# Performance work log

Hardware: AMD Instinct MI355X
Metric: run time of the kernel (lower is better)

Reference implementation:

```python
import jax, jax.numpy as jnp
import numpy as np

B, S, C = 32, 512, 512      # batch, seq_len, enc_in (n_vars, used as tokens)
D, DF, H, P, PRED, K = 512, 2048, 8, 16, 96, 10


def _pe(L, d):
    # standard sinusoidal positional embedding (Informer-style)
    pos = jnp.arange(L, dtype=jnp.float32)[:, None]
    div = jnp.exp(jnp.arange(0, d, 2, dtype=jnp.float32) * (-np.log(10000.0) / d))
    pe = jnp.zeros((L, d), dtype=jnp.float32)
    pe = pe.at[:, 0::2].set(jnp.sin(pos * div))
    pe = pe.at[:, 1::2].set(jnp.cos(pos * div))
    return pe


def _pwattn(x, qw, qb, kw, kb, vw, vb, ow, ob, seq_len, pred_len):
    # patchwise attention over P-sized patches of the feature dim
    N = x.shape[0]
    query = jax.nn.relu(x @ qw + qb)                       # (N, pred_len)
    q = query.reshape(N, pred_len // P, P)
    k = (x @ kw + kb).reshape(N, seq_len // P, P)
    v = jax.nn.relu(x @ vw + vb).reshape(N, seq_len // P, P)
    A = jax.nn.softmax(jnp.einsum('ble,bse->bls', q, k) / float(np.sqrt(P)), axis=-1)
    V = jnp.einsum('bls,bse->ble', A, v).reshape(N, pred_len)
    return query + V @ ow + ob


def setup_inputs():
    key = jax.random.key(0)
    ks = iter(jax.random.split(key, 48))
    w = lambda shape: jax.random.normal(next(ks), shape, dtype=jnp.float32) * 0.02
    z = lambda n: jnp.zeros((n,), dtype=jnp.float32)
    return {
        'x_enc': jax.random.normal(next(ks), (B, S, C), dtype=jnp.float32),
        'x_mark_enc': jax.random.normal(next(ks), (B, S, 4), dtype=jnp.float32),
        'x_dec': jax.random.normal(next(ks), (B, PRED, C), dtype=jnp.float32),
        'x_mark_dec': jax.random.normal(next(ks), (B, PRED, 4), dtype=jnp.float32),
        'embed_w': w((S, D)),
        'q_w': w((D, D)), 'q_b': z(D), 'k_w': w((D, D)), 'k_b': z(D),
        'v_w': w((D, D)), 'v_b': z(D), 'o_w': w((D, D)), 'o_b': z(D),
        'enc_w': w((D, D)), 'enc_b': z(D),
        'f1q_w': w((D, DF)), 'f1q_b': z(DF), 'f1k_w': w((D, D)), 'f1k_b': z(D),
        'f1v_w': w((D, D)), 'f1v_b': z(D), 'f1o_w': w((DF, DF)), 'f1o_b': z(DF),
        'f2q_w': w((DF, D)), 'f2q_b': z(D), 'f2k_w': w((DF, DF)), 'f2k_b': z(DF),
        'f2v_w': w((DF, DF)), 'f2v_b': z(DF), 'f2o_w': w((D, D)), 'f2o_b': z(D),
        'ln_g': jnp.ones((DF,), dtype=jnp.float32), 'ln_b': z(DF),
        'fc_w': w((D, PRED)), 'fc_b': z(PRED),
    }


def reference(x_enc, x_mark_enc, x_dec, x_mark_dec, embed_w,
              q_w, q_b, k_w, k_b, v_w, v_b, o_w, o_b, enc_w, enc_b,
              f1q_w, f1q_b, f1k_w, f1k_b, f1v_w, f1v_b, f1o_w, f1o_b,
              f2q_w, f2q_b, f2k_w, f2k_b, f2v_w, f2v_b, f2o_w, f2o_b,
              ln_g, ln_b, fc_w, fc_b):
    # instance norm over time dim (stats detached)
    mean = jax.lax.stop_gradient(jnp.mean(x_enc, axis=1, keepdims=True))
    x = x_enc - mean
    std = jax.lax.stop_gradient(jnp.sqrt(jnp.var(x, axis=1, keepdims=True) + 1e-5))
    x = x / std
    x = jnp.transpose(x, (0, 2, 1))                        # (B, C, S)
    emb = jax.nn.relu(x @ embed_w) + _pe(C, D)[None]       # (B, C, D)
    # GAttn: full scores -> per-row top-k mask -> softmax -> AV
    E = D // H
    q = jax.nn.relu(emb @ q_w + q_b).reshape(B, C, H, E)
    kk = (emb @ k_w + k_b).reshape(B, C, H, E)
    v = jax.nn.relu(emb @ v_w + v_b).reshape(B, C, H, E)
    scores = jnp.einsum('blhe,bshe->bhls', q, kk)          # (B, H, C, C)
    thr = jax.lax.top_k(scores, K)[0][..., -1:]
    scores = jnp.where(scores < thr, -jnp.inf, scores)
    A = jax.nn.softmax(scores / float(np.sqrt(E)), axis=-1)
    attn_out = jnp.einsum('bhls,bshd->blhd', A, v).reshape(B, C, D)
    y = emb + (attn_out @ o_w + o_b)
    y = jax.nn.leaky_relu(y, 0.5) @ enc_w + enc_b
    y = y.reshape(B * C, D)
    # PWattn FFN with LayerNorm in between
    h = jax.nn.elu(_pwattn(y, f1q_w, f1q_b, f1k_w, f1k_b, f1v_w, f1v_b, f1o_w, f1o_b, D, DF))
    mu = jnp.mean(h, axis=-1, keepdims=True)
    var = jnp.var(h, axis=-1, keepdims=True)
    h = (h - mu) / jnp.sqrt(var + 1e-5) * ln_g + ln_b
    y = _pwattn(h, f2q_w, f2q_b, f2k_w, f2k_b, f2v_w, f2v_b, f2o_w, f2o_b, DF, D)
    y = y.reshape(B, C, D)
    dec = y @ fc_w + fc_b                                   # (B, C, PRED)
    dec = jnp.transpose(dec, (0, 2, 1))                     # (B, PRED, C)
    dec = dec * std + mean
    return dec[:, -PRED:, :]
```

## Files before the change

### kernel.cpp

```cpp
#include <hip/hip_runtime.h>
#include <float.h>
#include <math.h>
#include <stdint.h>


#define NB   32
#define SS   512
#define CC   512
#define DD   512
#define DFF  2048
#define HH   8
#define EE   64
#define PRED 96

typedef __attribute__((ext_vector_type(8))) short short8;
typedef __attribute__((ext_vector_type(4))) float f32x4;

__device__ __forceinline__ float b2f(ushort u) {
  union { float f; uint32_t i; } c; c.i = ((uint32_t)u) << 16; return c.f;
}
__device__ __forceinline__ ushort f2b(float f) {
  union { float f; uint32_t i; } c; c.f = f;
  uint32_t x = c.i;
  return (ushort)((x + 0x7fffu + ((x >> 16) & 1u)) >> 16);
}
__device__ __forceinline__ float lin(const void* p, size_t i, int f32) {
  return f32 ? ((const float*)p)[i] : b2f(((const ushort*)p)[i]);
}
__device__ __forceinline__ void split_bf(float x, ushort& hi, ushort& lo) {
  hi = f2b(x);
  lo = f2b(x - b2f(hi));
}

template<int CTRL>
__device__ __forceinline__ float dppmov(float x) {
  union { float f; int i; } a, b;
  a.f = x;
  b.i = __builtin_amdgcn_update_dpp(a.i, a.i, CTRL, 0xF, 0xF, false);
  return b.f;
}
__device__ __forceinline__ float red16_max(float x) {
  x = fmaxf(x, dppmov<0xB1>(x));
  x = fmaxf(x, dppmov<0x4E>(x));
  x = fmaxf(x, dppmov<0x141>(x));
  x = fmaxf(x, dppmov<0x140>(x));
  return x;
}
__device__ __forceinline__ float red16_sum(float x) {
  x += dppmov<0xB1>(x);
  x += dppmov<0x4E>(x);
  x += dppmov<0x141>(x);
  x += dppmov<0x140>(x);
  return x;
}

__global__ __launch_bounds__(256) void detect_dtype(
    const ushort* __restrict__ x, int* __restrict__ flag)
{
  __shared__ float red[256];
  const int t = threadIdx.x;
  float v = fabsf(b2f(x[2 * t]));
  if (!(v < 1e30f)) v = 1e30f;
  red[t] = v;
  __syncthreads();
  for (int off = 128; off > 0; off >>= 1) {
    if (t < off) red[t] = fmaxf(red[t], red[t + off]);
    __syncthreads();
  }
  if (t == 0) flag[0] = (red[0] > 1e6f) ? 1 : 0;
}

__global__ __launch_bounds__(256) void instnorm_stats(
    const void* __restrict__ x, float* __restrict__ meanb, float* __restrict__ stdb,
    const int* __restrict__ dtf)
{
  const int f32 = *dtf;
  const int c = blockIdx.x * 256 + threadIdx.x;
  const int b = blockIdx.y;
  float s = 0.f, s2 = 0.f;
  for (int t = 0; t < SS; ++t) {
    const float xv = lin(x, ((size_t)(b * SS) + t) * CC + c, f32);
    s += xv; s2 += xv * xv;
  }
  const float mu  = s * (1.f / SS);
  const float var = s2 * (1.f / SS) - mu * mu;
  meanb[b * CC + c] = mu;
  stdb [b * CC + c] = sqrtf(var + 1e-5f);
}

__global__ __launch_bounds__(256) void norm_transpose(
    const void* __restrict__ x, const float* __restrict__ meanb,
    const float* __restrict__ stdb, float* __restrict__ xTc, int b_base,
    const int* __restrict__ dtf)
{
  const int f32 = *dtf;
  __shared__ float t[32][33];
  const int s0 = blockIdx.x * 32, c0 = blockIdx.y * 32, lb = blockIdx.z;
  const int b = b_base + lb;
  const int tx = threadIdx.x & 31, ty = threadIdx.x >> 5;
  #pragma unroll
  for (int i = 0; i < 4; ++i) {
    const int s = s0 + ty + i * 8;
    t[ty + i * 8][tx] = lin(x, ((size_t)(b * SS) + s) * CC + c0 + tx, f32);
  }
  __syncthreads();
  #pragma unroll
  for (int i = 0; i < 4; ++i) {
    const int c = c0 + ty + i * 8;
    const float mu = meanb[b * CC + c], sd = stdb[b * CC + c];
    xTc[((size_t)(lb * CC) + c) * SS + s0 + tx] = (t[tx][ty + i * 8] - mu) / sd;
  }
}

__global__ __launch_bounds__(256) void norm_transpose_split(
    const void* __restrict__ x, const float* __restrict__ meanb,
    const float* __restrict__ stdb, ushort* __restrict__ xh,
    ushort* __restrict__ xl, int b_base, const int* __restrict__ dtf)
{
  const int f32 = *dtf;
  __shared__ float t[32][33];
  const int s0 = blockIdx.x * 32, c0 = blockIdx.y * 32, lb = blockIdx.z;
  const int b = b_base + lb;
  const int tx = threadIdx.x & 31, ty = threadIdx.x >> 5;
  #pragma unroll
  for (int i = 0; i < 4; ++i) {
    const int s = s0 + ty + i * 8;
    t[ty + i * 8][tx] = lin(x, ((size_t)(b * SS) + s) * CC + c0 + tx, f32);
  }
  __syncthreads();
  #pragma unroll
  for (int i = 0; i < 4; ++i) {
    const int c = c0 + ty + i * 8;
    const float mu = meanb[b * CC + c], sd = stdb[b * CC + c];
    const float v = (t[tx][ty + i * 8] - mu) / sd;
    const size_t idx = ((size_t)(lb * CC) + c) * SS + s0 + tx;
    ushort hi, lo; split_bf(v, hi, lo);
    xh[idx] = hi; xl[idx] = lo;
  }
}

__global__ __launch_bounds__(256) void transpose_w(
    const void* __restrict__ W, ushort* __restrict__ Wt, int K, int N,
    const int* __restrict__ dtf)
{
  const int f32 = *dtf;
  __shared__ float t[32][33];
  const int n0 = blockIdx.x * 32, k0 = blockIdx.y * 32;
  const int tx = threadIdx.x & 31, ty = threadIdx.x >> 5;
  #pragma unroll
  for (int i = 0; i < 4; ++i)
    t[ty + i * 8][tx] = lin(W, (size_t)(k0 + ty + i * 8) * N + n0 + tx, f32);
  __syncthreads();
  #pragma unroll
  for (int i = 0; i < 4; ++i)
    Wt[(size_t)(n0 + ty + i * 8) * K + k0 + tx] = f2b(t[tx][ty + i * 8]);
}

__global__ __launch_bounds__(256) void transpose_w_split(
    const void* __restrict__ W, ushort* __restrict__ Whi, ushort* __restrict__ Wlo,
    int K, int N, const int* __restrict__ dtf)
{
  const int f32 = *dtf;
  __shared__ float t[32][33];
  const int n0 = blockIdx.x * 32, k0 = blockIdx.y * 32;
  const int tx = threadIdx.x & 31, ty = threadIdx.x >> 5;
  #pragma unroll
  for (int i = 0; i < 4; ++i)
    t[ty + i * 8][tx] = lin(W, (size_t)(k0 + ty + i * 8) * N + n0 + tx, f32);
  __syncthreads();
  #pragma unroll
  for (int i = 0; i < 4; ++i) {
    const size_t idx = (size_t)(n0 + ty + i * 8) * K + k0 + tx;
    ushort hi, lo; split_bf(t[tx][ty + i * 8], hi, lo);
    Whi[idx] = hi; Wlo[idx] = lo;
  }
}

enum GemmMode { M_BIAS = 0, M_BIAS_RELU = 1, M_RELU_PE = 2,
                M_ADD_BIAS_LEAKY = 3, M_ADD_BIAS_ELU = 4, M_ADD_BIAS = 5,
                M_ADD2_BIAS_LEAKY = 6 };

template<typename AT, typename ADT, typename OT, int MODE>
__global__ __launch_bounds__(256) void gemm_kernel(
    const AT* __restrict__ A, const void* __restrict__ Bw,
    const void* __restrict__ bias, const ADT* __restrict__ addend,
    OT* __restrict__ Cout, int M, int K, int Nn, const int* __restrict__ dtf)
{
  const int f32 = *dtf;
  __shared__ __align__(16) float As[16][68];
  __shared__ __align__(16) float Bs[16][68];
  const int tid = threadIdx.x;
  const int m0 = blockIdx.y * 64, n0 = blockIdx.x * 64;
  const int tx = tid & 15, ty = tid >> 4;
  const int la_m = tid >> 2, la_k = (tid & 3) * 4;
  const int lb_k = tid >> 4, lb_n = (tid & 15) * 4;
  float acc[4][4];
  #pragma unroll
  for (int i = 0; i < 4; ++i)
    #pragma unroll
    for (int j = 0; j < 4; ++j) acc[i][j] = 0.f;
  const size_t a_row = (size_t)(m0 + la_m) * K;

  for (int k0 = 0; k0 < K; k0 += 16) {
    if constexpr (sizeof(AT) == 4) {
      const float4 av = *reinterpret_cast<const float4*>(A + a_row + k0 + la_k);
      As[la_k + 0][la_m] = av.x; As[la_k + 1][la_m] = av.y;
      As[la_k + 2][la_m] = av.z; As[la_k + 3][la_m] = av.w;
    } else {
      const ushort4 av = *reinterpret_cast<const ushort4*>(A + a_row + k0 + la_k);
      As[la_k + 0][la_m] = b2f(av.x); As[la_k + 1][la_m] = b2f(av.y);
      As[la_k + 2][la_m] = b2f(av.z); As[la_k + 3][la_m] = b2f(av.w);
    }
    {
      const size_t boff = (size_t)(k0 + lb_k) * Nn + n0 + lb_n;
      if (f32) {
        const float4 bv = *reinterpret_cast<const float4*>((const float*)Bw + boff);
        Bs[lb_k][lb_n + 0] = bv.x; Bs[lb_k][lb_n + 1] = bv.y;
        Bs[lb_k][lb_n + 2] = bv.z; Bs[lb_k][lb_n + 3] = bv.w;
      } else {
        const ushort4 bv = *reinterpret_cast<const ushort4*>((const ushort*)Bw + boff);
        Bs[lb_k][lb_n + 0] = b2f(bv.x); Bs[lb_k][lb_n + 1] = b2f(bv.y);
        Bs[lb_k][lb_n + 2] = b2f(bv.z); Bs[lb_k][lb_n + 3] = b2f(bv.w);
      }
    }
    __syncthreads();
    #pragma unroll
    for (int k = 0; k < 16; ++k) {
      const float4 a4 = *reinterpret_cast<const float4*>(&As[k][ty * 4]);
      const float4 b4 = *reinterpret_cast<const float4*>(&Bs[k][tx * 4]);
      const float aa[4] = {a4.x, a4.y, a4.z, a4.w};
      const float bb[4] = {b4.x, b4.y, b4.z, b4.w};
      #pragma unroll
      for (int i = 0; i < 4; ++i)
        #pragma unroll
        for (int j = 0; j < 4; ++j)
          acc[i][j] = fmaf(aa[i], bb[j], acc[i][j]);
    }
    __syncthreads();
  }

  float biasv[4];
  if constexpr (MODE != M_RELU_PE) {
    #pragma unroll
    for (int j = 0; j < 4; ++j) biasv[j] = lin(bias, n0 + tx * 4 + j, f32);
  }
  #pragma unroll
  for (int i = 0; i < 4; ++i) {
    const int m = m0 + ty * 4 + i;
    #pragma unroll
    for (int j = 0; j < 4; ++j) {
      const int n = n0 + tx * 4 + j;
      float v = acc[i][j];
      if constexpr (MODE == M_BIAS) {
        v += biasv[j];
      } else if constexpr (MODE == M_BIAS_RELU) {
        v = fmaxf(v + biasv[j], 0.f);
      } else if constexpr (MODE == M_RELU_PE) {
        v = fmaxf(v, 0.f);
        const float freq = expf((float)(n & ~1) * (-0.017988946f));
        const float ang  = (float)(m & (CC - 1)) * freq;
        v += (n & 1) ? cosf(ang) : sinf(ang);
      } else {
        float ad;
        if constexpr (sizeof(ADT) == 4) ad = ((const float*)addend)[(size_t)m * Nn + n];
        else                            ad = b2f(((const ushort*)addend)[(size_t)m * Nn + n]);
        v = ad + v + biasv[j];
        if constexpr (MODE == M_ADD_BIAS_LEAKY) v = (v >= 0.f) ? v : 0.5f * v;
        else if constexpr (MODE == M_ADD_BIAS_ELU) v = (v > 0.f) ? v : expm1f(v);
      }
      if constexpr (sizeof(OT) == 4) ((float*)Cout)[(size_t)m * Nn + n] = v;
      else                           ((ushort*)Cout)[(size_t)m * Nn + n] = f2b(v);
    }
  }
}

template<typename AT, typename ADT, typename OT, int MODE>
static void launch_gemm(const void* A, const void* Bw, const void* bias, const void* add,
                        void* Cout, int M, int K, int Nn, const int* dtf, hipStream_t stream)
{
  dim3 grid(Nn / 64, M / 64);
  gemm_kernel<AT, ADT, OT, MODE><<<grid, dim3(256), 0, stream>>>(
      (const AT*)A, Bw, bias, (const ADT*)add, (OT*)Cout, M, K, Nn, dtf);
}

template<typename ADT, typename OT, int MODE>
__global__ __launch_bounds__(256) void mgemm_kernel(
    const ushort* __restrict__ A, const ushort* __restrict__ Wt,
    const void* __restrict__ bias, const ADT* __restrict__ addend,
    const ushort* __restrict__ addend2,
    OT* __restrict__ Cout, int M, int K, int Nn, const int* __restrict__ dtf)
{
  const int f32 = *dtf;
  __shared__ __align__(16) ushort As[128][40];
  __shared__ __align__(16) ushort Bs[128][40];
  const int tid = threadIdx.x;
  const int m0 = blockIdx.y * 128, n0 = blockIdx.x * 128;
  const int wave = tid >> 6, lane = tid & 63;
  const int wm = wave & 1, wn = wave >> 1;
  const int quad = lane >> 4, l15 = lane & 15;

  f32x4 acc[4][4];
  #pragma unroll
  for (int i = 0; i < 4; ++i)
    #pragma unroll
    for (int j = 0; j < 4; ++j) acc[i][j] = (f32x4){0.f, 0.f, 0.f, 0.f};

  const int srow = tid >> 1, sseg = (tid & 1) * 16;
  const size_t a_base = (size_t)(m0 + srow) * K + sseg;
  const size_t b_base = (size_t)(n0 + srow) * K + sseg;

  for (int k0 = 0; k0 < K; k0 += 32) {
    {
      const float4* ga = reinterpret_cast<const float4*>(A + a_base + k0);
      const float4* gb = reinterpret_cast<const float4*>(Wt + b_base + k0);
      const float4 a0 = ga[0], a1 = ga[1];
      const float4 b0 = gb[0], b1 = gb[1];
      float4* da = reinterpret_cast<float4*>(&As[srow][sseg]);
      float4* db = reinterpret_cast<float4*>(&Bs[srow][sseg]);
      da[0] = a0; da[1] = a1;
      db[0] = b0; db[1] = b1;
    }
    __syncthreads();
    short8 af[4], bf[4];
    #pragma unroll
    for (int i = 0; i < 4; ++i)
      af[i] = *reinterpret_cast<const short8*>(&As[wm * 64 + i * 16 + l15][quad * 8]);
    #pragma unroll
    for (int j = 0; j < 4; ++j)
      bf[j] = *reinterpret_cast<const short8*>(&Bs[wn * 64 + j * 16 + l15][quad * 8]);
    #pragma unroll
    for (int i = 0; i < 4; ++i)
      #pragma unroll
      for (int j = 0; j < 4; ++j)
        acc[i][j] = __builtin_amdgcn_mfma_f32_16x16x32_bf16(af[i], bf[j], acc[i][j], 0, 0, 0);
    __syncthreads();
  }

  #pragma unroll
  for (int j = 0; j < 4; ++j) {
    const int n = n0 + wn * 64 + j * 16 + l15;
    const float bv = lin(bias, n, f32);
    #pragma unroll
    for (int i = 0; i < 4; ++i) {
      #pragma unroll
      for (int r = 0; r < 4; ++r) {
        const int m = m0 + wm * 64 + i * 16 + quad * 4 + r;
        float v = acc[i][j][r];
        if constexpr (MODE == M_BIAS) {
          v += bv;
        } else if constexpr (MODE == M_BIAS_RELU) {
          v = fmaxf(v + bv, 0.f);
        } else if constexpr (MODE == M_ADD2_BIAS_LEAKY) {
          const size_t ix = (size_t)m * Nn + n;
          const float ad = b2f(((const ushort*)addend)[ix]) + b2f(addend2[ix]);
          v = ad + v + bv;
          v = (v >= 0.f) ? v : 0.5f * v;
        } else {
          float ad;
          if constexpr (sizeof(ADT) == 4) ad = ((const float*)addend)[(size_t)m * Nn + n];
          else                            ad = b2f(((const ushort*)addend)[(size_t)m * Nn + n]);
          v = ad + v + bv;
          if constexpr (MODE == M_ADD_BIAS_ELU)   v = (v > 0.f) ? v : expm1f(v);
          else if constexpr (MODE == M_ADD_BIAS_LEAKY) v = (v >= 0.f) ? v : 0.5f * v;
        }
        if constexpr (sizeof(OT) == 4) ((float*)Cout)[(size_t)m * Nn + n] = v;
        else                           ((ushort*)Cout)[(size_t)m * Nn + n] = f2b(v);
      }
    }
  }
}

template<typename ADT, typename OT, int MODE>
static void launch_mgemm(const void* A, const void* Wt, const void* bias, const void* add,
                         void* Cout, int M, int K, int Nn, const int* dtf, hipStream_t stream,
                         const void* add2 = nullptr)
{
  dim3 grid(Nn / 128, M / 128);
  mgemm_kernel<ADT, OT, MODE><<<grid, dim3(256), 0, stream>>>(
      (const ushort*)A, (const ushort*)Wt, bias, (const ADT*)add, (const ushort*)add2,
      (OT*)Cout, M, K, Nn, dtf);
}

template<typename ADT, typename OT, int MODE>
__global__ __launch_bounds__(256) void mgemm64_kernel(
    const ushort* __restrict__ A, const ushort* __restrict__ Wt,
    const void* __restrict__ bias, const ADT* __restrict__ addend,
    const ushort* __restrict__ addend2,
    OT* __restrict__ Cout, int M, int K, int Nn, const int* __restrict__ dtf)
{
  const int f32 = *dtf;
  __shared__ __align__(16) ushort As[64][40];
  __shared__ __align__(16) ushort Bs[64][40];
  const int tid = threadIdx.x;
  const int m0 = blockIdx.y * 64, n0 = blockIdx.x * 64;
  const int wave = tid >> 6, lane = tid & 63;
  const int wm = wave & 1, wn = wave >> 1;
  const int quad = lane >> 4, l15 = lane & 15;

  f32x4 acc[2][2];
  #pragma unroll
  for (int i = 0; i < 2; ++i)
    #pragma unroll
    for (int j = 0; j < 2; ++j) acc[i][j] = (f32x4){0.f, 0.f, 0.f, 0.f};

  const int srow = tid >> 2, sseg = (tid & 3) * 8;
  const size_t a_base = (size_t)(m0 + srow) * K + sseg;
  const size_t b_base = (size_t)(n0 + srow) * K + sseg;

  for (int k0 = 0; k0 < K; k0 += 32) {
    *reinterpret_cast<float4*>(&As[srow][sseg]) =
        *reinterpret_cast<const float4*>(A + a_base + k0);
    *reinterpret_cast<float4*>(&Bs[srow][sseg]) =
        *reinterpret_cast<const float4*>(Wt + b_base + k0);
    __syncthreads();
    short8 af[2], bf[2];
    #pragma unroll
    for (int i = 0; i < 2; ++i) {
      af[i] = *reinterpret_cast<const short8*>(&As[wm * 32 + i * 16 + l15][quad * 8]);
      bf[i] = *reinterpret_cast<const short8*>(&Bs[wn * 32 + i * 16 + l15][quad * 8]);
    }
    #pragma unroll
    for (int i = 0; i < 2; ++i)
      #pragma unroll
      for (int j = 0; j < 2; ++j)
        acc[i][j] = __builtin_amdgcn_mfma_f32_16x16x32_bf16(af[i], bf[j], acc[i][j], 0, 0, 0);
    __syncthreads();
  }

  #pragma unroll
  for (int j = 0; j < 2; ++j) {
    const int n = n0 + wn * 32 + j * 16 + l15;
    const float bv = lin(bias, n, f32);
    #pragma unroll
    for (int i = 0; i < 2; ++i) {
      #pragma unroll
      for (int r = 0; r < 4; ++r) {
        const int m = m0 + wm * 32 + i * 16 + quad * 4 + r;
        float v = acc[i][j][r];
        if constexpr (MODE == M_BIAS) {
          v += bv;
        } else if constexpr (MODE == M_BIAS_RELU) {
          v = fmaxf(v + bv, 0.f);
        } else if constexpr (MODE == M_ADD2_BIAS_LEAKY) {
          const size_t ix = (size_t)m * Nn + n;
          const float ad = b2f(((const ushort*)addend)[ix]) + b2f(addend2[ix]);
          v = ad + v + bv;
          v = (v >= 0.f) ? v : 0.5f * v;
        } else {
          float ad;
          if constexpr (sizeof(ADT) == 4) ad = ((const float*)addend)[(size_t)m * Nn + n];
          else                            ad = b2f(((const ushort*)addend)[(size_t)m * Nn + n]);
          v = ad + v + bv;
          if constexpr (MODE == M_ADD_BIAS_ELU)   v = (v > 0.f) ? v : expm1f(v);
          else if constexpr (MODE == M_ADD_BIAS_LEAKY) v = (v >= 0.f) ? v : 0.5f * v;
        }
        if constexpr (sizeof(OT) == 4) ((float*)Cout)[(size_t)m * Nn + n] = v;
        else                           ((ushort*)Cout)[(size_t)m * Nn + n] = f2b(v);
      }
    }
  }
}

template<typename ADT, typename OT, int MODE>
static void launch_mgemm64(const void* A, const void* Wt, const void* bias, const void* add,
                           void* Cout, int M, int K, int Nn, const int* dtf, hipStream_t stream,
                           const void* add2 = nullptr)
{
  dim3 grid(Nn / 64, M / 64);
  mgemm64_kernel<ADT, OT, MODE><<<grid, dim3(256), 0, stream>>>(
      (const ushort*)A, (const ushort*)Wt, bias, (const ADT*)add, (const ushort*)add2,
      (OT*)Cout, M, K, Nn, dtf);
}

enum Epi3 { E3_RELU_PE = 0, E3_RELU_SPLIT = 1, E3_SPLIT = 2, E3_RELU_VT = 3 };

template<int EPI>
__global__ __launch_bounds__(256) void mgemm3_kernel(
    const ushort* __restrict__ Ah, const ushort* __restrict__ Al,
    const ushort* __restrict__ Bh, const ushort* __restrict__ Bl,
    const void* __restrict__ bias,
    ushort* __restrict__ Oh, ushort* __restrict__ Ol,
    int M, int K, int Nn, const int* __restrict__ dtf)
{
  const int f32 = *dtf;
  __shared__ __align__(16) ushort AsH[64][40];
  __shared__ __align__(16) ushort AsL[64][40];
  __shared__ __align__(16) ushort BsH[64][40];
  __shared__ __align__(16) ushort BsL[64][40];
  const int tid = threadIdx.x;
  const int m0 = blockIdx.y * 64, n0 = blockIdx.x * 64;
  const int wave = tid >> 6, lane = tid & 63;
  const int wm = wave & 1, wn = wave >> 1;
  const int quad = lane >> 4, l15 = lane & 15;

  f32x4 acc[2][2];
  #pragma unroll
  for (int i = 0; i < 2; ++i)
    #pragma unroll
    for (int j = 0; j < 2; ++j) acc[i][j] = (f32x4){0.f, 0.f, 0.f, 0.f};

  const int srow = tid >> 2, sseg = (tid & 3) * 8;
  const size_t a_base = (size_t)(m0 + srow) * K + sseg;
  const size_t b_base = (size_t)(n0 + srow) * K + sseg;

  for (int k0 = 0; k0 < K; k0 += 32) {
    *reinterpret_cast<float4*>(&AsH[srow][sseg]) =
        *reinterpret_cast<const float4*>(Ah + a_base + k0);
    *reinterpret_cast<float4*>(&AsL[srow][sseg]) =
        *reinterpret_cast<const float4*>(Al + a_base + k0);
    *reinterpret_cast<float4*>(&BsH[srow][sseg]) =
        *reinterpret_cast<const float4*>(Bh + b_base + k0);
    *reinterpret_cast<float4*>(&BsL[srow][sseg]) =
        *reinterpret_cast<const float4*>(Bl + b_base + k0);
    __syncthreads();
    short8 afh[2], afl[2], bfh[2], bfl[2];
    #pragma unroll
    for (int i = 0; i < 2; ++i) {
      afh[i] = *reinterpret_cast<const short8*>(&AsH[wm * 32 + i * 16 + l15][quad * 8]);
      afl[i] = *reinterpret_cast<const short8*>(&AsL[wm * 32 + i * 16 + l15][quad * 8]);
      bfh[i] = *reinterpret_cast<const short8*>(&BsH[wn * 32 + i * 16 + l15][quad * 8]);
      bfl[i] = *reinterpret_cast<const short8*>(&BsL[wn * 32 + i * 16 + l15][quad * 8]);
    }
    #pragma unroll
    for (int i = 0; i < 2; ++i)
      #pragma unroll
      for (int j = 0; j < 2; ++j) {
        acc[i][j] = __builtin_amdgcn_mfma_f32_16x16x32_bf16(afh[i], bfh[j], acc[i][j], 0, 0, 0);
        acc[i][j] = __builtin_amdgcn_mfma_f32_16x16x32_bf16(afh[i], bfl[j], acc[i][j], 0, 0, 0);
        acc[i][j] = __builtin_amdgcn_mfma_f32_16x16x32_bf16(afl[i], bfh[j], acc[i][j], 0, 0, 0);
      }
    __syncthreads();
  }

  #pragma unroll
  for (int j = 0; j < 2; ++j) {
    const int n = n0 + wn * 32 + j * 16 + l15;
    float bv = 0.f;
    if constexpr (EPI != E3_RELU_PE) bv = lin(bias, n, f32);
    #pragma unroll
    for (int i = 0; i < 2; ++i) {
      #pragma unroll
      for (int r = 0; r < 4; ++r) {
        const int m = m0 + wm * 32 + i * 16 + quad * 4 + r;
        float v = acc[i][j][r];
        if constexpr (EPI == E3_RELU_PE) {
          v = fmaxf(v, 0.f);
          const float freq = expf((float)(n & ~1) * (-0.017988946f));
          const float ang  = (float)(m & (CC - 1)) * freq;
          v += (n & 1) ? cosf(ang) : sinf(ang);
        } else if constexpr (EPI == E3_RELU_SPLIT || EPI == E3_RELU_VT) {
          v = fmaxf(v + bv, 0.f);
        } else {
          v = v + bv;
        }
        if constexpr (EPI == E3_RELU_VT) {
          Oh[((size_t)((m >> 9) * 512 + n)) * 512 + (m & 511)] = f2b(v);
        } else {
          ushort hi, lo; split_bf(v, hi, lo);
          Oh[(size_t)m * Nn + n] = hi;
          Ol[(size_t)m * Nn + n] = lo;
        }
      }
    }
  }
}

template<int EPI>
static void launch_mgemm3(const void* Ahv, const void* Alv, const ushort* Bh,
                          const ushort* Bl, const void* bias, void* Oh, void* Ol,
                          int M, int K, int Nn, const int* dtf, hipStream_t stream)
{
  dim3 grid(Nn / 64, M / 64);
  mgemm3_kernel<EPI><<<grid, dim3(256), 0, stream>>>(
      (const ushort*)Ahv, (const ushort*)Alv, Bh, Bl, bias,
      (ushort*)Oh, (ushort*)Ol, M, K, Nn, dtf);
}

__global__ __launch_bounds__(256, 4) void gattn_mfma(
    const ushort* __restrict__ qsh, const ushort* __restrict__ qsl,
    const ushort* __restrict__ ksh, const ushort* __restrict__ ksl,
    const ushort* __restrict__ vt, ushort* __restrict__ out)
{
  const int tid = threadIdx.x;
  const int wave = tid >> 6, lane = tid & 63;
  const int quad = lane >> 4, l15 = lane & 15;
  const int l0 = blockIdx.x * 16;
  const int h = blockIdx.y, bz = blockIdx.z;

  __shared__ __align__(16) ushort P[16][520];
  __shared__ float cand[16][40];
  __shared__ float psum[16][4];

  short8 ah[2], al[2];
  {
    const size_t qoff = ((size_t)bz * CC + l0 + l15) * DD + h * EE + quad * 8;
    ah[0] = *reinterpret_cast<const short8*>(qsh + qoff);
    ah[1] = *reinterpret_cast<const short8*>(qsh + qoff + 32);
    al[0] = *reinterpret_cast<const short8*>(qsl + qoff);
    al[1] = *reinterpret_cast<const short8*>(qsl + qoff + 32);
  }

  f32x4 sacc[8];
  {
    const size_t kbase = ((size_t)bz * CC + wave * 16 + l15) * DD + h * EE + quad * 8;
    #pragma unroll
    for (int c = 0; c < 8; ++c) {
      f32x4 acc = (f32x4){0.f, 0.f, 0.f, 0.f};
      #pragma unroll
      for (int kk = 0; kk < 2; ++kk) {
        const size_t off = kbase + (size_t)(c * 64) * DD + kk * 32;
        const short8 bh = *reinterpret_cast<const short8*>(ksh + off);
        const short8 bl = *reinterpret_cast<const short8*>(ksl + off);
        acc = __builtin_amdgcn_mfma_f32_16x16x32_bf16(ah[kk], bh, acc, 0, 0, 0);
        acc = __builtin_amdgcn_mfma_f32_16x16x32_bf16(ah[kk], bl, acc, 0, 0, 0);
        acc = __builtin_amdgcn_mfma_f32_16x16x32_bf16(al[kk], bh, acc, 0, 0, 0);
      }
      sacc[c] = acc;
    }
  }

  #pragma unroll
  for (int r = 0; r < 4; ++r) {
    float wk[8];
    #pragma unroll
    for (int c = 0; c < 8; ++c) wk[c] = sacc[c][r];
    float myg = 0.f;
    for (int it = 0; it < 10; ++it) {
      float lm = wk[0];
      #pragma unroll
      for (int c = 1; c < 8; ++c) lm = fmaxf(lm, wk[c]);
      const float gm = red16_max(lm);
      if (l15 == it) myg = gm;
      if (it < 9) {
        const unsigned long long msk = __ballot(lm == gm);
        const int sel = (__ffsll((unsigned long long)((msk >> (quad * 16)) & 0xFFFFull)) - 1)
                        + quad * 16;
        if (lane == sel) {
          #pragma unroll
          for (int c = 0; c < 8; ++c) { if (wk[c] == gm) { wk[c] = -FLT_MAX; break; } }
        }
      }
    }
    if (l15 < 10) cand[quad * 4 + r][wave * 10 + l15] = myg;
  }
  __syncthreads();

  float mx, thr;
  {
    const int mr = lane & 15;
    float h0 = cand[mr][0], h1 = cand[mr][10], h2 = cand[mr][20], h3 = cand[mr][30];
    int i0 = 0, i1 = 0, i2 = 0, i3 = 0;
    float cur = 0.f;
    mx = 0.f;
    #pragma unroll
    for (int t = 0; t < 10; ++t) {
      cur = fmaxf(fmaxf(h0, h1), fmaxf(h2, h3));
      if (t == 0) mx = cur;
      if (t < 9) {
        const bool a0 = (cur == h0);
        const bool a1 = !a0 && (cur == h1);
        const bool a2 = !a0 && !a1 && (cur == h2);
        const int ni0 = i0 + (a0 ? 1 : 0);
        const int ni1 = i1 + (a1 ? 1 : 0);
        const int ni2 = i2 + (a2 ? 1 : 0);
        const int ni3 = i3 + ((a0 || a1 || a2) ? 0 : 1);
        const int off = a0 ? ni0 : (a1 ? 10 + ni1 : (a2 ? 20 + ni2 : 30 + ni3));
        const float nv = cand[mr][off];
        h0 = a0 ? nv : h0;
        h1 = a1 ? nv : h1;
        h2 = a2 ? nv : h2;
        h3 = (a0 || a1 || a2) ? h3 : nv;
        i0 = ni0; i1 = ni1; i2 = ni2; i3 = ni3;
      }
    }
    thr = cur;
  }
  float thrR[4], mxR[4];
  #pragma unroll
  for (int r = 0; r < 4; ++r) {
    thrR[r] = __shfl(thr, quad * 4 + r);
    mxR[r]  = __shfl(mx,  quad * 4 + r);
  }

  #pragma unroll
  for (int r = 0; r < 4; ++r) {
    const int Rr = quad * 4 + r;
    float s = 0.f;
    #pragma unroll
    for (int c = 0; c < 8; ++c) {
      const float sc = sacc[c][r];
      const float p = (sc >= thrR[r]) ? expf((sc - mxR[r]) * 0.125f) : 0.f;
      P[Rr][c * 64 + wave * 16 + l15] = f2b(p);
      s += p;
    }
    s = red16_sum(s);
    if (l15 == 0) psum[Rr][wave] = s;
  }
  __syncthreads();

  f32x4 pacc = (f32x4){0.f, 0.f, 0.f, 0.f};
  const size_t vbase = ((size_t)bz * 512 + h * EE + wave * 16 + l15) * 512 + quad * 8;
  #pragma unroll
  for (int c = 0; c < 4; ++c) {
    #pragma unroll
    for (int ks = 0; ks < 4; ++ks) {
      const int s0 = c * 128 + ks * 32;
      const short8 pa = *reinterpret_cast<const short8*>(&P[l15][s0 + quad * 8]);
      const short8 vb = *reinterpret_cast<const short8*>(vt + vbase + s0);
      pacc = __builtin_amdgcn_mfma_f32_16x16x32_bf16(pa, vb, pacc, 0, 0, 0);
    }
  }

  #pragma unroll
  for (int r = 0; r < 4; ++r) {
    const int Rr = quad * 4 + r;
    const float4 ps = *reinterpret_cast<const float4*>(&psum[Rr][0]);
    const float inv = 1.f / (ps.x + ps.y + ps.z + ps.w);
    out[((size_t)bz * CC + l0 + Rr) * DD + h * EE + wave * 16 + l15] = f2b(pacc[r] * inv);
  }
}

template<typename OT>
// ... 162 lines not shown
{
  const int tid = threadIdx.x;
  const int wave = tid >> 6, lane = tid & 63;
  const int quad = lane >> 4, l15 = lane & 15;
  const int n = blockIdx.x * 4 + wave;

  __shared__ __align__(16) ushort Pl[4][16][136];

  const float*  qrow = query2 + (size_t)n * 512;
  const ushort* krow = k2 + (size_t)n * DFF;
  const ushort* vrow = v2 + (size_t)n * DFF;
  ushort* orow = V2 + (size_t)n * 512;

  const short8 zz = {0, 0, 0, 0, 0, 0, 0, 0};
  const f32x4 zacc = (f32x4){0.f, 0.f, 0.f, 0.f};

  short8 kb[8];
  #pragma unroll
  for (int nt = 0; nt < 8; ++nt)
    kb[nt] = (quad < 2)
        ? *reinterpret_cast<const short8*>(krow + (nt * 16 + l15) * 16 + quad * 8)
        : zz;

  short8 vb[4];
  #pragma unroll
  for (int kt = 0; kt < 4; ++kt)
    #pragma unroll
    for (int i = 0; i < 8; ++i)
      vb[kt][i] = (short)vrow[(kt * 32 + quad * 8 + i) * 16 + l15];

  #pragma unroll
  for (int mt = 0; mt < 2; ++mt) {
    short8 ahh = zz, all_ = zz;
    if (quad < 2) {
      const float* qp = qrow + (mt * 16 + l15) * 16 + quad * 8;
      #pragma unroll
      for (int i = 0; i < 8; ++i) {
        ushort hi_, lo_; split_bf(qp[i], hi_, lo_);
        ahh[i] = (short)hi_; all_[i] = (short)lo_;
      }
    }
    f32x4 acc[8];
    #pragma unroll
    for (int nt = 0; nt < 8; ++nt) {
      f32x4 t = __builtin_amdgcn_mfma_f32_16x16x32_bf16(all_, kb[nt], zacc, 0, 0, 0);
      acc[nt] = __builtin_amdgcn_mfma_f32_16x16x32_bf16(ahh, kb[nt], t, 0, 0, 0);
    }
    float inv[4];
    #pragma unroll
    for (int r = 0; r < 4; ++r) {
      float m = acc[0][r];
      #pragma unroll
      for (int nt = 1; nt < 8; ++nt) m = fmaxf(m, acc[nt][r]);
      m = red16_max(m);
      float s = 0.f;
      #pragma unroll
      for (int nt = 0; nt < 8; ++nt) {
        const float p = expf((acc[nt][r] - m) * 0.25f);
        acc[nt][r] = p; s += p;
      }
      s = red16_sum(s);
      inv[r] = 1.f / s;
    }
    #pragma unroll
    for (int nt = 0; nt < 8; ++nt)
      #pragma unroll
      for (int r = 0; r < 4; ++r)
        Pl[wave][quad * 4 + r][nt * 16 + l15] = f2b(acc[nt][r]);
    f32x4 pv = zacc;
    #pragma unroll
    for (int kt = 0; kt < 4; ++kt) {
      const short8 pa = *reinterpret_cast<const short8*>(&Pl[wave][l15][kt * 32 + quad * 8]);
      pv = __builtin_amdgcn_mfma_f32_16x16x32_bf16(pa, vb[kt], pv, 0, 0, 0);
    }
    #pragma unroll
    for (int r = 0; r < 4; ++r)
      orow[(mt * 16 + quad * 4 + r) * 16 + l15] = f2b(pv[r] * inv[r]);
  }
}

__global__ __launch_bounds__(128) void pwattn1_kernel(
    const ushort* __restrict__ query, const float* __restrict__ k1,
    const float* __restrict__ v1, ushort* __restrict__ V1)
{
  const int n = blockIdx.x, tid = threadIdx.x;
  __shared__ float ks[512], vs[512];
  __shared__ float Am[128][33];
  for (int i = tid; i < 512; i += 128) { ks[i] = k1[(size_t)n * 512 + i]; vs[i] = v1[(size_t)n * 512 + i]; }
  __syncthreads();
  {
    const int l = tid;
    float qv[16];
    const ushort* qp = query + (size_t)n * DFF + l * 16;
    #pragma unroll
    for (int e = 0; e < 16; ++e) qv[e] = b2f(qp[e]);
    float scl[32], mx = -FLT_MAX;
    #pragma unroll
    for (int s = 0; s < 32; ++s) {
      float a = 0.f;
      #pragma unroll
      for (int e = 0; e < 16; ++e) a += qv[e] * ks[s * 16 + e];
      scl[s] = a; mx = fmaxf(mx, a);
    }
    float sum = 0.f;
    #pragma unroll
    for (int s = 0; s < 32; ++s) { const float p = expf((scl[s] - mx) * 0.25f); scl[s] = p; sum += p; }
    const float invs = 1.f / sum;
    #pragma unroll
    for (int s = 0; s < 32; ++s) Am[l][s] = scl[s] * invs;
  }
  __syncthreads();
  #pragma unroll
  for (int r = 0; r < 16; ++r) {
    const int idx = tid + 128 * r;
    const int l = idx >> 4, e = idx & 15;
    float a = 0.f;
    #pragma unroll
    for (int s = 0; s < 32; ++s) a += Am[l][s] * vs[s * 16 + e];
    V1[(size_t)n * DFF + idx] = f2b(a);
  }
}

__global__ __launch_bounds__(256) void ln_kernel(
    ushort* __restrict__ h, const void* __restrict__ g, const void* __restrict__ bt,
    const int* __restrict__ dtf)
{
  const int f32 = *dtf;
  const int n = blockIdx.x, tid = threadIdx.x;
  ushort* hp = h + (size_t)n * DFF;
  float x[8]; float s = 0.f, s2 = 0.f;
  #pragma unroll
  for (int i = 0; i < 8; ++i) {
    const float xv = b2f(hp[tid + 256 * i]);
    x[i] = xv; s += xv; s2 += xv * xv;
  }
  __shared__ float rs[256], rq[256];
  rs[tid] = s; rq[tid] = s2;
  __syncthreads();
  for (int off = 128; off > 0; off >>= 1) {
    if (tid < off) { rs[tid] += rs[tid + off]; rq[tid] += rq[tid + off]; }
    __syncthreads();
  }
  const float mu  = rs[0] * (1.f / DFF);
  const float var = rq[0] * (1.f / DFF) - mu * mu;
  const float inv = rsqrtf(var + 1e-5f);
  #pragma unroll
  for (int i = 0; i < 8; ++i) {
    const int d = tid + 256 * i;
    hp[d] = f2b((x[i] - mu) * inv * lin(g, d, f32) + lin(bt, d, f32));
  }
}

template<typename OT>
__global__ __launch_bounds__(128) void pwattn2_kernel(
    const float* __restrict__ query2, const ushort* __restrict__ k2,
    const ushort* __restrict__ v2, OT* __restrict__ V2)
{
  const int n = blockIdx.x, tid = threadIdx.x;
  __shared__ float ks[2048], vs[2048];
  __shared__ float Am[32][129];
  for (int i = tid; i < 2048; i += 128) {
    ks[i] = b2f(k2[(size_t)n * DFF + i]);
    vs[i] = b2f(v2[(size_t)n * DFF + i]);
  }
  __syncthreads();
  if (tid < 32) {
    const int l = tid;
    float qv[16];
    #pragma unroll
    for (int e = 0; e < 16; ++e) qv[e] = query2[(size_t)n * 512 + l * 16 + e];
    float mx = -FLT_MAX;
    for (int s = 0; s < 128; ++s) {
      float a = 0.f;
      #pragma unroll
      for (int e = 0; e < 16; ++e) a += qv[e] * ks[s * 16 + e];
      Am[l][s] = a; mx = fmaxf(mx, a);
    }
    float sum = 0.f;
    for (int s = 0; s < 128; ++s) { const float p = expf((Am[l][s] - mx) * 0.25f); Am[l][s] = p; sum += p; }
    const float invs = 1.f / sum;
    for (int s = 0; s < 128; ++s) Am[l][s] *= invs;
  }
  __syncthreads();
  #pragma unroll
  for (int r = 0; r < 4; ++r) {
    const int idx = tid + 128 * r;
    const int l = idx >> 4, e = idx & 15;
    float a = 0.f;
    for (int s = 0; s < 128; ++s) a += Am[l][s] * vs[s * 16 + e];
    if constexpr (sizeof(OT) == 4) V2[(size_t)n * 512 + idx] = a;
    else                           V2[(size_t)n * 512 + idx] = f2b(a);
  }
}

__global__ __launch_bounds__(128) void final_kernel(
    const float* __restrict__ y, const void* __restrict__ fc_w,
    const void* __restrict__ fc_b, const float* __restrict__ meanb,
    const float* __restrict__ stdb, void* __restrict__ out, int row_base,
    const int* __restrict__ dtf)
{
  const int f32 = *dtf;
  const int row = row_base + blockIdx.x;
  const int b = row >> 9, c = row & 511;
  const int tid = threadIdx.x;
  __shared__ float yr[512];
  for (int i = tid; i < 512; i += 128) yr[i] = y[(size_t)blockIdx.x * 512 + i];
  __syncthreads();
  if (tid < PRED) {
    float a = 0.f;
    for (int d = 0; d < 512; ++d) a += yr[d] * lin(fc_w, d * PRED + tid, f32);
    a += lin(fc_b, tid, f32);
    const float r = a * stdb[row] + meanb[row];
    const size_t oi = ((size_t)b * PRED + tid) * CC + c;
    if (f32) ((float*)out)[oi] = r;
    else     ((ushort*)out)[oi] = f2b(r);
  }
}

extern "C" void kernel_launch(void* const* d_in, const int* in_sizes, int n_in,
                              void* d_out, int out_size, void* d_ws, size_t ws_size,
                              hipStream_t stream)
{
  (void)in_sizes; (void)n_in; (void)out_size;
  const void* x_enc   = d_in[0];
  const void* embed_w = d_in[4];
  const void* q_w = d_in[5],  * q_b = d_in[6];
  const void* k_w = d_in[7],  * k_b = d_in[8];
  const void* v_w = d_in[9],  * v_b = d_in[10];
  const void* o_w = d_in[11], * o_b = d_in[12];
  const void* enc_w = d_in[13], * enc_b = d_in[14];
  const void* f1q_w = d_in[15], * f1q_b = d_in[16];
  const void* f1k_w = d_in[17], * f1k_b = d_in[18];
  const void* f1v_w = d_in[19], * f1v_b = d_in[20];
  const void* f1o_w = d_in[21], * f1o_b = d_in[22];
  const void* f2q_w = d_in[23], * f2q_b = d_in[24];
  const void* f2k_w = d_in[25], * f2k_b = d_in[26];
  const void* f2v_w = d_in[27], * f2v_b = d_in[28];
  const void* f2o_w = d_in[29], * f2o_b = d_in[30];
  const void* ln_g  = d_in[31], * ln_b  = d_in[32];
  const void* fc_w  = d_in[33], * fc_b  = d_in[34];

  const size_t HDR = 131072 + 1024;
  const size_t E_F1Q = 512ull * 2048, E_F1O = 2048ull * 2048, E_F2Q = 2048ull * 512;
  const size_t E_F2K = 2048ull * 2048, E_F2V = 2048ull * 2048, E_F2O = 512ull * 512;
  const size_t E_SQ  = 512ull * 512;
  const size_t WT_EL = E_F1Q + E_F1O + E_F2Q + E_F2K + E_F2V + E_F2O + 4 * E_SQ + 8 * E_SQ;
  const size_t WT_BYTES = WT_EL * 2;
  const size_t PB_MFMA = 4ull * 512 * 512 * 4 + 3ull * 512 * DFF * 2;
  const size_t PB_FB   = 5ull * 512 * 512 * 4 + 3ull * 512 * DFF * 2;

  const int use_mfma = (HDR + WT_BYTES + PB_MFMA <= ws_size) ? 1 : 0;
  const size_t PER_BATCH = use_mfma ? PB_MFMA : PB_FB;
  const size_t FIXED = HDR + (use_mfma ? WT_BYTES : 0);
  int BPC = 1;
  for (int c = 8; c >= 1; c >>= 1) {
    if (FIXED + (size_t)c * PER_BATCH <= ws_size) { BPC = c; break; }
  }
  const int R = BPC * 512;

  char* ws = (char*)d_ws;
  float* meanb = (float*)ws;
  float* stdb  = (float*)(ws + 65536);
  int*   dtf   = (int*)(ws + 131072);
  ushort* wt_base = (ushort*)(ws + HDR);
  ushort* wt_f1q = wt_base;
  ushort* wt_f1o = wt_f1q + E_F1Q;
  ushort* wt_f2q = wt_f1o + E_F1O;
  ushort* wt_f2k = wt_f2q + E_F2Q;
  ushort* wt_f2v = wt_f2k + E_F2K;
  ushort* wt_f2o = wt_f2v + E_F2V;
  ushort* wt_o   = wt_f2o + E_F2O;
  ushort* wt_enc = wt_o   + E_SQ;
  ushort* wt_f1k = wt_enc + E_SQ;
  ushort* wt_f1v = wt_f1k + E_SQ;
  ushort* wt_embh = wt_f1v + E_SQ;
  ushort* wt_embl = wt_embh + E_SQ;
  ushort* wt_qh   = wt_embl + E_SQ;
  ushort* wt_ql   = wt_qh   + E_SQ;
  ushort* wt_kh   = wt_ql   + E_SQ;
  ushort* wt_kl   = wt_kh   + E_SQ;
  ushort* wt_vh   = wt_kl   + E_SQ;
  ushort* wt_vl   = wt_vh   + E_SQ;

  char* arena = ws + FIXED;
  const size_t FSL = (size_t)R * 512 * 4;
  const size_t GSL = (size_t)R * DFF * 2;
  void* A_ = arena;
  void* B_ = arena + FSL;
  void* C_ = arena + 2 * FSL;
  void* D_ = arena + 3 * FSL;
  void* E_ = arena + 4 * FSL;
  char* gb = arena + (size_t)(use_mfma ? 4 : 5) * FSL;
  void* G1 = gb;
  void* G2 = gb + GSL;
  void* G3 = gb + 2 * GSL;

  ushort* xTh  = (ushort*)G1; ushort* xTl  = xTh  + (size_t)R * 512;
  ushort* embh = (ushort*)G2; ushort* embl = embh + (size_t)R * 512;
  ushort* qsh  = (ushort*)C_; ushort* qsl  = qsh  + (size_t)R * 512;
  ushort* ksh  = (ushort*)D_; ushort* ksl  = ksh  + (size_t)R * 512;
  ushort* vt   = (ushort*)B_;

  detect_dtype<<<1, 256, 0, stream>>>((const ushort*)x_enc, dtf);
  instnorm_stats<<<dim3(2, NB), 256, 0, stream>>>(x_enc, meanb, stdb, dtf);

  if (use_mfma) {
    transpose_w<<<dim3(DFF / 32, 512 / 32), 256, 0, stream>>>(f1q_w, wt_f1q, 512, DFF, dtf);
    transpose_w<<<dim3(DFF / 32, DFF / 32), 256, 0, stream>>>(f1o_w, wt_f1o, DFF, DFF, dtf);
    transpose_w<<<dim3(512 / 32, DFF / 32), 256, 0, stream>>>(f2q_w, wt_f2q, DFF, 512, dtf);
    transpose_w<<<dim3(DFF / 32, DFF / 32), 256, 0, stream>>>(f2k_w, wt_f2k, DFF, DFF, dtf);
    transpose_w<<<dim3(DFF / 32, DFF / 32), 256, 0, stream>>>(f2v_w, wt_f2v, DFF, DFF, dtf);
    transpose_w<<<dim3(512 / 32, 512 / 32), 256, 0, stream>>>(f2o_w, wt_f2o, 512, 512, dtf);
    transpose_w<<<dim3(512 / 32, 512 / 32), 256, 0, stream>>>(o_w,   wt_o,   512, 512, dtf);
    transpose_w<<<dim3(512 / 32, 512 / 32), 256, 0, stream>>>(enc_w, wt_enc, 512, 512, dtf);
    transpose_w<<<dim3(512 / 32, 512 / 32), 256, 0, stream>>>(f1k_w, wt_f1k, 512, 512, dtf);
    transpose_w<<<dim3(512 / 32, 512 / 32), 256, 0, stream>>>(f1v_w, wt_f1v, 512, 512, dtf);
    transpose_w_split<<<dim3(512 / 32, 512 / 32), 256, 0, stream>>>(embed_w, wt_embh, wt_embl, 512, 512, dtf);
    transpose_w_split<<<dim3(512 / 32, 512 / 32), 256, 0, stream>>>(q_w, wt_qh, wt_ql, 512, 512, dtf);
    transpose_w_split<<<dim3(512 / 32, 512 / 32), 256, 0, stream>>>(k_w, wt_kh, wt_kl, 512, 512, dtf);
    transpose_w_split<<<dim3(512 / 32, 512 / 32), 256, 0, stream>>>(v_w, wt_vh, wt_vl, 512, 512, dtf);
  }

  for (int bc = 0; bc < NB / BPC; ++bc) {
    const int b0 = bc * BPC;
    if (use_mfma) {
      norm_transpose_split<<<dim3(16, 16, BPC), 256, 0, stream>>>(
          x_enc, meanb, stdb, xTh, xTl, b0, dtf);
      launch_mgemm3<E3_RELU_PE>(xTh, xTl, wt_embh, wt_embl, nullptr,
                                embh, embl, R, 512, 512, dtf, stream);
      launch_mgemm3<E3_RELU_SPLIT>(embh, embl, wt_qh, wt_ql, q_b,
                                   qsh, qsl, R, 512, 512, dtf, stream);
      launch_mgemm3<E3_SPLIT>(embh, embl, wt_kh, wt_kl, k_b,
                              ksh, ksl, R, 512, 512, dtf, stream);
      launch_mgemm3<E3_RELU_VT>(embh, embl, wt_vh, wt_vl, v_b,
                                vt, nullptr, R, 512, 512, dtf, stream);
      gattn_mfma<<<dim3(CC / 16, HH, BPC), 256, 0, stream>>>(
          qsh, qsl, ksh, ksl, vt, (ushort*)A_);
      launch_mgemm64<ushort, ushort, M_ADD2_BIAS_LEAKY>(
          A_, wt_o, o_b, embh, C_, R, 512, 512, dtf, stream, embl);
      launch_mgemm64<float, ushort, M_BIAS>(C_, wt_enc, enc_b, nullptr, D_, R, 512, 512, dtf, stream);
      launch_mgemm<float, ushort, M_BIAS_RELU>(D_, wt_f1q, f1q_b, nullptr, G1, R, 512, DFF, dtf, stream);
      launch_mgemm64<float, float, M_BIAS     >(D_, wt_f1k, f1k_b, nullptr, A_, R, 512, 512, dtf, stream);
      launch_mgemm64<float, float, M_BIAS_RELU>(D_, wt_f1v, f1v_b, nullptr, B_, R, 512, 512, dtf, stream);
      pwattn1_mfma<<<R / 4, 256, 0, stream>>>(
          (const ushort*)G1, (const float*)A_, (const float*)B_, (ushort*)G2);
      launch_mgemm<ushort, ushort, M_ADD_BIAS_ELU>(G2, wt_f1o, f1o_b, G1, G1, R, DFF, DFF, dtf, stream);
      ln_kernel<<<R, 256, 0, stream>>>((ushort*)G1, ln_g, ln_b, dtf);
      launch_mgemm64<float, float, M_BIAS_RELU>(G1, wt_f2q, f2q_b, nullptr, A_, R, DFF, 512, dtf, stream);
      launch_mgemm<float, ushort, M_BIAS     >(G1, wt_f2k, f2k_b, nullptr, G2, R, DFF, DFF, dtf, stream);
      launch_mgemm<float, ushort, M_BIAS_RELU>(G1, wt_f2v, f2v_b, nullptr, G3, R, DFF, DFF, dtf, stream);
      pwattn2_mfma<<<R / 4, 256, 0, stream>>>(
          (const float*)A_, (const ushort*)G2, (const ushort*)G3, (ushort*)B_);
      launch_mgemm64<float, float, M_ADD_BIAS>(B_, wt_f2o, f2o_b, A_, C_, R, 512, 512, dtf, stream);
    } else {
      norm_transpose<<<dim3(16, 16, BPC), 256, 0, stream>>>(x_enc, meanb, stdb, (float*)A_, b0, dtf);
      launch_gemm<float, float, float, M_RELU_PE >(A_, embed_w, nullptr, nullptr, B_, R, 512, 512, dtf, stream);
      launch_gemm<float, float, float, M_BIAS_RELU>(B_, q_w, q_b, nullptr, C_, R, 512, 512, dtf, stream);
      launch_gemm<float, float, float, M_BIAS     >(B_, k_w, k_b, nullptr, D_, R, 512, 512, dtf, stream);
      launch_gemm<float, float, float, M_BIAS_RELU>(B_, v_w, v_b, nullptr, E_, R, 512, 512, dtf, stream);
      gattn_fb<float><<<dim3(CC / 4, HH, BPC), 256, 0, stream>>>(
          (float*)C_, (float*)D_, (float*)E_, (float*)A_);
      launch_gemm<float, float, float, M_ADD_BIAS_LEAKY>(A_, o_w, o_b, B_, C_, R, 512, 512, dtf, stream);
      launch_gemm<float, float, float, M_BIAS>(C_, enc_w, enc_b, nullptr, D_, R, 512, 512, dtf, stream);
      launch_gemm<float, float, ushort, M_BIAS_RELU>(D_, f1q_w, f1q_b, nullptr, G1, R, 512, DFF, dtf, stream);
      launch_gemm<float, float, float,  M_BIAS     >(D_, f1k_w, f1k_b, nullptr, A_, R, 512, 512, dtf, stream);
      launch_gemm<float, float, float,  M_BIAS_RELU>(D_, f1v_w, f1v_b, nullptr, B_, R, 512, 512, dtf, stream);
      pwattn1_kernel<<<R, 128, 0, stream>>>((const ushort*)G1, (const float*)A_, (const float*)B_, (ushort*)G2);
      launch_gemm<ushort, ushort, ushort, M_ADD_BIAS_ELU>(G2, f1o_w, f1o_b, G1, G1, R, DFF, DFF, dtf, stream);
      ln_kernel<<<R, 256, 0, stream>>>((ushort*)G1, ln_g, ln_b, dtf);
      launch_gemm<ushort, float, float,  M_BIAS_RELU>(G1, f2q_w, f2q_b, nullptr, A_, R, DFF, 512, dtf, stream);
      launch_gemm<ushort, float, ushort, M_BIAS     >(G1, f2k_w, f2k_b, nullptr, G2, R, DFF, DFF, dtf, stream);
      launch_gemm<ushort, float, ushort, M_BIAS_RELU>(G1, f2v_w, f2v_b, nullptr, G3, R, DFF, DFF, dtf, stream);
      pwattn2_kernel<float><<<R, 128, 0, stream>>>((const float*)A_, (const ushort*)G2, (const ushort*)G3, (float*)B_);
      launch_gemm<float, float, float, M_ADD_BIAS>(B_, f2o_w, f2o_b, A_, C_, R, 512, 512, dtf, stream);
    }
    final_kernel<<<R, 128, 0, stream>>>((const float*)C_, fc_w, fc_b, meanb, stdb, d_out, b0 * 512, dtf);
  }
}
```

Before: 2.584 ms.

## Use direct global-to-LDS loads with XOR swizzle in MFMA GEMMs; split instnorm stats

The two bf16 MFMA GEMM kernels now stage A and B tiles with global_load_lds (direct global-to-LDS DMA) instead of loading through registers, and drop the 40-element padding in favour of an XOR swizzle on the 16-byte segment to avoid LDS bank conflicts. The instance-norm statistics kernel is split into a partial-sum kernel parallelised over 8 time chunks and a small reduce kernel, giving far more blocks than the previous 64. Scratch arena buffers A_ and B_ are reused for the partial sums, which relies on them not holding live data at that point.

```diff
diff --git a/kernel.cpp b/kernel.cpp
--- a/kernel.cpp
+++ b/kernel.cpp
@@ -31,6 +31,11 @@
   hi = f2b(x);
   lo = f2b(x - b2f(hi));
 }
+__device__ __forceinline__ void gl_lds16(const void* g, void* l) {
+  __builtin_amdgcn_global_load_lds(
+      (const __attribute__((address_space(1))) void*)g,
+      (__attribute__((address_space(3))) void*)l, 16, 0, 0);
+}
 
 template<int CTRL>
 __device__ __forceinline__ float dppmov(float x) {
@@ -70,17 +75,34 @@
   if (t == 0) flag[0] = (red[0] > 1e6f) ? 1 : 0;
 }
 
-__global__ __launch_bounds__(256) void instnorm_stats(
-    const void* __restrict__ x, float* __restrict__ meanb, float* __restrict__ stdb,
+__global__ __launch_bounds__(256) void instnorm_partial(
+    const void* __restrict__ x, float* __restrict__ ps, float* __restrict__ pq,
     const int* __restrict__ dtf)
 {
   const int f32 = *dtf;
   const int c = blockIdx.x * 256 + threadIdx.x;
   const int b = blockIdx.y;
+  const int t0 = blockIdx.z * 64;
   float s = 0.f, s2 = 0.f;
-  for (int t = 0; t < SS; ++t) {
+  for (int t = t0; t < t0 + 64; ++t) {
     const float xv = lin(x, ((size_t)(b * SS) + t) * CC + c, f32);
     s += xv; s2 += xv * xv;
+  }
+  const int pidx = (b * 8 + blockIdx.z) * CC + c;
+  ps[pidx] = s; pq[pidx] = s2;
+}
+
+__global__ __launch_bounds__(256) void instnorm_reduce(
+    const float* __restrict__ ps, const float* __restrict__ pq,
+    float* __restrict__ meanb, float* __restrict__ stdb)
+{
+  const int c = blockIdx.x * 256 + threadIdx.x;
+  const int b = blockIdx.y;
+  float s = 0.f, s2 = 0.f;
+  #pragma unroll
+  for (int i = 0; i < 8; ++i) {
+    s  += ps[(b * 8 + i) * CC + c];
+    s2 += pq[(b * 8 + i) * CC + c];
   }
   const float mu  = s * (1.f / SS);
   const float var = s2 * (1.f / SS) - mu * mu;
@@ -291,8 +313,8 @@
     OT* __restrict__ Cout, int M, int K, int Nn, const int* __restrict__ dtf)
 {
   const int f32 = *dtf;
-  __shared__ __align__(16) ushort As[128][40];
-  __shared__ __align__(16) ushort Bs[128][40];
+  __shared__ __align__(16) ushort As[128][32];
+  __shared__ __align__(16) ushort Bs[128][32];
   const int tid = threadIdx.x;
   const int m0 = blockIdx.y * 128, n0 = blockIdx.x * 128;
   const int wave = tid >> 6, lane = tid & 63;
@@ -305,29 +327,26 @@
     #pragma unroll
     for (int j = 0; j < 4; ++j) acc[i][j] = (f32x4){0.f, 0.f, 0.f, 0.f};
 
-  const int srow = tid >> 1, sseg = (tid & 1) * 16;
-  const size_t a_base = (size_t)(m0 + srow) * K + sseg;
-  const size_t b_base = (size_t)(n0 + srow) * K + sseg;
+  const int srow_l = lane >> 2;
+  const int slot   = lane & 3;
 
   for (int k0 = 0; k0 < K; k0 += 32) {
-    {
-      const float4* ga = reinterpret_cast<const float4*>(A + a_base + k0);
-      const float4* gb = reinterpret_cast<const float4*>(Wt + b_base + k0);
-      const float4 a0 = ga[0], a1 = ga[1];
-      const float4 b0 = gb[0], b1 = gb[1];
-      float4* da = reinterpret_cast<float4*>(&As[srow][sseg]);
-      float4* db = reinterpret_cast<float4*>(&Bs[srow][sseg]);
-      da[0] = a0; da[1] = a1;
-      db[0] = b0; db[1] = b1;
+    #pragma unroll
+    for (int i = 0; i < 2; ++i) {
+      const int row = wave * 32 + i * 16 + srow_l;
+      const int sseg = (slot ^ ((row >> 1) & 3)) * 8;
+      gl_lds16(A  + (size_t)(m0 + row) * K + k0 + sseg, &As[wave * 32 + i * 16][0]);
+      gl_lds16(Wt + (size_t)(n0 + row) * K + k0 + sseg, &Bs[wave * 32 + i * 16][0]);
     }
     __syncthreads();
     short8 af[4], bf[4];
     #pragma unroll
-    for (int i = 0; i < 4; ++i)
-      af[i] = *reinterpret_cast<const short8*>(&As[wm * 64 + i * 16 + l15][quad * 8]);
-    #pragma unroll
-    for (int j = 0; j < 4; ++j)
-      bf[j] = *reinterpret_cast<const short8*>(&Bs[wn * 64 + j * 16 + l15][quad * 8]);
+    for (int i = 0; i < 4; ++i) {
+      const int ra = wm * 64 + i * 16 + l15;
+      af[i] = *reinterpret_cast<const short8*>(&As[ra][(quad ^ ((ra >> 1) & 3)) * 8]);
+      const int rb = wn * 64 + i * 16 + l15;
+      bf[i] = *reinterpret_cast<const short8*>(&Bs[rb][(quad ^ ((rb >> 1) & 3)) * 8]);
+    }
     #pragma unroll
     for (int i = 0; i < 4; ++i)
       #pragma unroll
@@ -389,8 +408,8 @@
     OT* __restrict__ Cout, int M, int K, int Nn, const int* __restrict__ dtf)
 {
   const int f32 = *dtf;
-  __shared__ __align__(16) ushort As[64][40];
-  __shared__ __align__(16) ushort Bs[64][40];
+  __shared__ __align__(16) ushort As[64][32];
+  __shared__ __align__(16) ushort Bs[64][32];
   const int tid = threadIdx.x;
   const int m0 = blockIdx.y * 64, n0 = blockIdx.x * 64;
   const int wave = tid >> 6, lane = tid & 63;
@@ -403,21 +422,24 @@
     #pragma unroll
     for (int j = 0; j < 2; ++j) acc[i][j] = (f32x4){0.f, 0.f, 0.f, 0.f};
 
-  const int srow = tid >> 2, sseg = (tid & 3) * 8;
-  const size_t a_base = (size_t)(m0 + srow) * K + sseg;
-  const size_t b_base = (size_t)(n0 + srow) * K + sseg;
+  const int srow_l = lane >> 2;
+  const int slot   = lane & 3;
 
   for (int k0 = 0; k0 < K; k0 += 32) {
-    *reinterpret_cast<float4*>(&As[srow][sseg]) =
-        *reinterpret_cast<const float4*>(A + a_base + k0);
-    *reinterpret_cast<float4*>(&Bs[srow][sseg]) =
-        *reinterpret_cast<const float4*>(Wt + b_base + k0);
+    {
+      const int row = wave * 16 + srow_l;
+      const int sseg = (slot ^ ((row >> 1) & 3)) * 8;
+      gl_lds16(A  + (size_t)(m0 + row) * K + k0 + sseg, &As[wave * 16][0]);
+      gl_lds16(Wt + (size_t)(n0 + row) * K + k0 + sseg, &Bs[wave * 16][0]);
+    }
     __syncthreads();
     short8 af[2], bf[2];
     #pragma unroll
     for (int i = 0; i < 2; ++i) {
-      af[i] = *reinterpret_cast<const short8*>(&As[wm * 32 + i * 16 + l15][quad * 8]);
-      bf[i] = *reinterpret_cast<const short8*>(&Bs[wn * 32 + i * 16 + l15][quad * 8]);
+      const int ra = wm * 32 + i * 16 + l15;
+      af[i] = *reinterpret_cast<const short8*>(&As[ra][(quad ^ ((ra >> 1) & 3)) * 8]);
+      const int rb = wn * 32 + i * 16 + l15;
+      bf[i] = *reinterpret_cast<const short8*>(&Bs[rb][(quad ^ ((rb >> 1) & 3)) * 8]);
     }
     #pragma unroll
     for (int i = 0; i < 2; ++i)
@@ -1186,7 +1208,10 @@
   ushort* vt   = (ushort*)B_;
 
   detect_dtype<<<1, 256, 0, stream>>>((const ushort*)x_enc, dtf);
-  instnorm_stats<<<dim3(2, NB), 256, 0, stream>>>(x_enc, meanb, stdb, dtf);
+  instnorm_partial<<<dim3(2, NB, 8), 256, 0, stream>>>(
+      x_enc, (float*)A_, (float*)B_, dtf);
+  instnorm_reduce<<<dim3(2, NB), 256, 0, stream>>>(
+      (const float*)A_, (const float*)B_, meanb, stdb);
 
   if (use_mfma) {
     transpose_w<<<dim3(DFF / 32, 512 / 32), 256, 0, stream>>>(f1q_w, wt_f1q, 512, DFF, dtf);
```

After: 2.872 ms. 1.11x slower.
